# Kernel optimization log

Hardware: AMD Instinct MI355X
Metric: run time of the kernel (lower is better)

Reference implementation:

```python
import jax, jax.numpy as jnp
import numpy as np
from jax import lax

MU = 3.986004418e14   # Earth GM [m^3/s^2]
A_REF = 6378136.3     # reference radius [m]


def _constants(N, dtype):
    """Precompute n1/n2 normalization tables, diagonal aBar values and the
    sub-diagonal coefficient, exactly as in compute_normalization_constants
    and the first loop of compute_aBar (these depend only on N, not on data)."""
    L = N + 2
    l = np.arange(L, dtype=np.float64)[:, None]
    m = np.arange(L, dtype=np.float64)[None, :]
    mask = l >= m + 2
    d1 = np.where(mask, (l - m) * (l + m), 1.0)
    n1 = np.where(mask, np.sqrt((2.0 * l + 1.0) * (2.0 * l - 1.0) / d1), 0.0)
    d2 = np.where(mask, (l + m) * (l - m) * (2.0 * l - 3.0), 1.0)
    num2 = np.where(mask, (l + m - 1.0) * (2.0 * l + 1.0) * (l - m - 1.0), 0.0)
    n2 = np.where(mask, np.sqrt(num2 / d2), 0.0)
    # getK(0)=1, getK(l>0)=2
    k = np.where(np.arange(L) == 0, 1.0, 2.0)
    ls = np.arange(1, L, dtype=np.float64)
    f = np.ones(L)
    f[1:] = np.sqrt((2.0 * ls + 1.0) * k[1:] / (2.0 * ls * k[:-1]))
    diag = np.cumprod(f)                  # aBar[l,l]
    sub = np.zeros(L)
    sub[1:] = np.sqrt(2.0 * ls * k[:-1] / k[1:])  # aBar[l,l-1] = sub[l]*diag[l]*u
    cast = lambda x: jnp.asarray(x, dtype=dtype)
    return cast(n1), cast(n2), cast(diag), cast(sub)


def _forward(inputs, cBar, sBar):
    N = cBar.shape[0] - 3
    L = N + 2
    dt = inputs.dtype
    r, s, t, u = inputs[:, 0], inputs[:, 1], inputs[:, 2], inputs[:, 3]
    B = r.shape[0]
    n1, n2, diag, sub = _constants(N, dt)

    # rhol[b, l] = (mu/r) * (a/r)^l  for l = 0..N  (compute_rhol)
    rho = A_REF / r
    rhol = (MU / r)[:, None] * rho[:, None] ** jnp.arange(N + 1, dtype=dt)  # [B, N+1]

    # rE[m] + i*iM[m] = (s + i t)^m, m = 0..N+1  (compute_rE_iM)
    def trig_step(c, _):
        re, im = c
        nc = (s * re - t * im, s * im + t * re)
        return nc, nc
    init = (jnp.ones_like(s), jnp.zeros_like(s))
    _, (reS, imS) = lax.scan(trig_step, init, None, length=L - 1)
    rE = jnp.concatenate([init[0][None], reS], axis=0).T  # [B, L]
    iM = jnp.concatenate([init[1][None], imS], axis=0).T  # [B, L]

    # rows of aBar for l=0 and l=1
    sqrt3 = jnp.sqrt(jnp.asarray(3.0, dt))
    row0 = jnp.zeros((B, L), dt).at[:, 0].set(1.0)
    row1 = jnp.zeros((B, L), dt).at[:, 1].set(sqrt3)
    row1 = row1.at[:, 0].set(sqrt3 * u)  # aBar[1,0] = sub[1]*diag[1]*u

    cB = cBar[:, :L].astype(dt)
    sB = sBar[:, :L].astype(dt)
    eye = jnp.eye(L, dtype=dt)

    # scan over degree l = 2..N; carry = (aBar row l-1, aBar row l-2)
    xs = (n1[2:N + 1], n2[2:N + 1], cB[2:N + 1], sB[2:N + 1],
          eye[2:N + 1], eye[1:N], diag[2:N + 1], sub[2:N + 1],
          rhol[:, 2:N + 1].T)

    def body(carry, x):
        rl1, rl2 = carry
        n1l, n2l, cl, sl, el, elm1, dl, sbl, rh = x
        # recurrence a[l,m] = u*n1[l,m]*a[l-1,m] - n2[l,m]*a[l-2,m]  (m <= l-2;
        # n1/n2 are zero elsewhere so other entries stay 0 before diag fill)
        row = u[:, None] * (n1l * rl1) - n2l * rl2
        row = row + dl * el + (sbl * dl) * u[:, None] * elm1
        contrib = rh * jnp.sum(row * (cl * rE + sl * iM), axis=1)
        return (row, rl1), contrib

    _, contribs = lax.scan(body, (row1, row0), xs)  # [N-1, B]

    pot1 = rhol[:, 1] * jnp.sum(row1 * (cB[1] * rE + sB[1] * iM), axis=1)
    potential = MU / r + pot1 + contribs.sum(axis=0)
    return (-potential)[:, None]


def setup_inputs() -> dict:
    key = jax.random.key(0)
    B, N = 65536, 64
    k1, k2, k3, k4 = jax.random.split(key, 4)
    d = jax.random.normal(k1, (B, 3), dtype=jnp.float32)
    d = d / jnp.linalg.norm(d, axis=1, keepdims=True)  # (s,t,u) direction cosines
    r = A_REF * (1.0 + jax.random.uniform(k2, (B,), dtype=jnp.float32,
                                          minval=0.05, maxval=1.0))
    inputs = jnp.concatenate([r[:, None], d], axis=1)  # [B,4] = (r,s,t,u)
    cBar = jax.random.normal(k3, (N + 3, N + 3), dtype=jnp.float32) * 1e-3
    sBar = jax.random.normal(k4, (N + 3, N + 3), dtype=jnp.float32) * 1e-3
    return {"inputs": inputs, "cBar": cBar, "sBar": sBar}


def reference(inputs, cBar, sBar):
    return _forward(inputs, cBar, sBar)
```

## Files before the change

### kernel.cpp

```cpp
#include <hip/hip_runtime.h>
#include <math.h>

#define NDEG 64
#define LDCB 67

#define MU_F   398600441800000.0f
#define AREF_F 6378136.3f

#define NSUB 8
#define EPW  64
#define SGRP 72
#define NREC 9

struct Cons4 { float4 v[4]; };

__device__ __forceinline__ double n1d(int l, int m) {
    return sqrt((2.0 * l + 1.0) * (2.0 * l - 1.0) / ((double)(l - m) * (l + m)));
}
__device__ __forceinline__ double n2d(int l, int m) {
    return sqrt(((double)(l + m - 1) * (2 * l + 1) * (l - m - 1)) /
                ((double)(l + m) * (l - m) * (2 * l - 3)));
}

__global__ void pines_setup(const float* __restrict__ cBar,
                            const float* __restrict__ sBar,
                            float4* __restrict__ stream,
                            float4* __restrict__ hrec) {
    int tid = blockIdx.x * blockDim.x + threadIdx.x;
    if (tid < 8 * SGRP * 4) {
        int j = tid / (SGRP * 4);
        int rem = tid % (SGRP * 4);
        int d1 = 15 - 2 * j, d2 = 1 + 2 * j;
        int m = j, base = 0, idx = -1;
        for (int k = 0; k < 8; ++k) {
            int len  = 63 - m;
            int ecap = ((len + 7) >> 3) << 3;
            if (rem < base + ecap) { idx = rem - base; break; }
            base += ecap;
            m += (k & 1) ? d2 : d1;
        }
        float4 v = make_float4(0.0f, 0.0f, 0.0f, 0.0f);
        if (idx >= 0) {
            int l = m + 2 + idx;
            if (l <= NDEG) {
                double g = 1.0;
                for (int t2 = m + 2; t2 <= l; ++t2) g *= n1d(t2, m);
                double nn1   = n1d(l, m);
                double nprev = (l - 1 >= m + 2) ? n1d(l - 1, m) : 1.0;
                double nt2   = n2d(l, m) / (nn1 * nprev);
                v = make_float4((float)nt2,
                                (float)(g * (double)cBar[l * LDCB + m]),
                                (float)(g * (double)sBar[l * LDCB + m]),
                                0.0f);
            }
        }
        stream[tid] = v;
    } else {
        int h = tid - 8 * SGRP * 4;
        if (h < 8 * NREC) {
            int j = h / NREC, k = h % NREC;
            int d1 = 15 - 2 * j, d2 = 1 + 2 * j;
            int m = j;
            for (int kk = 0; kk < k; ++kk) m += (kk & 1) ? d2 : d1;
            float4 a = make_float4(0.0f, 0.0f, 0.0f, 0.0f);
            float4 b = make_float4(0.0f, 0.0f, 0.0f, 0.0f);
            if (m <= NDEG) {
                double diag = 1.0;
                for (int l = 1; l <= m; ++l) {
                    double kp = (l == 1) ? 1.0 : 2.0;
                    diag *= sqrt((2.0 * l + 1.0) * 2.0 / (2.0 * l * kp));
                }
                double sd = 0.0;
                if (m < NDEG) {
                    double kprev = (m == 0) ? 1.0 : 2.0;
                    double f    = sqrt((2.0 * (m + 1) + 1.0) * 2.0 /
                                       (2.0 * (m + 1) * kprev));
                    double sub1 = sqrt((double)(m + 1) * kprev);
                    sd = sub1 * diag * f;
                }
                float cmm = (m >= 1) ? cBar[m * LDCB + m] : 0.0f;
                float smm = (m >= 1) ? sBar[m * LDCB + m] : 0.0f;
                float cb1 = (m < NDEG) ? cBar[(m + 1) * LDCB + m] : 0.0f;
                float sb1 = (m < NDEG) ? sBar[(m + 1) * LDCB + m] : 0.0f;
                a = make_float4((float)diag, (float)sd, cmm, smm);
                b = make_float4(cb1, sb1, 0.0f, 0.0f);
            }
            hrec[h * 2]     = a;
            hrec[h * 2 + 1] = b;
        }
    }
}

__global__ __launch_bounds__(512, 8) void pines_kernel(
        const float4* __restrict__ inputs,
        const float4* __restrict__ stream,
        const float4* __restrict__ hrec,
        float* __restrict__ out, int B) {
    __shared__ float part[NSUB][EPW];

    int t = threadIdx.x;
    int j = __builtin_amdgcn_readfirstlane(t >> 6);
    int e = t & (EPW - 1);
    int elem = blockIdx.x * EPW + e;
    int lelem = elem < B ? elem : (B - 1);

    float4 in = inputs[lelem];
    float r = in.x, ss = in.y, tt = in.z, u = in.w;

    float rho   = AREF_F / r;
    float rho2  = rho * rho;
    float nrho2 = -rho2;
    float ur    = u * rho;

    int d1 = 15 - 2 * j;
    int d2 = 1 + 2 * j;

    auto cpow = [&](int e_, float& re_, float& im_) {
        float br = ss, bi = tt;
        re_ = 1.0f; im_ = 0.0f;
        int ee = e_;
        while (ee) {
            if (ee & 1) {
                float nr = re_ * br - im_ * bi;
                im_ = re_ * bi + im_ * br;
                re_ = nr;
            }
            float sr = br * br - bi * bi;
            bi = 2.0f * br * bi;
            br = sr;
            ee >>= 1;
        }
    };
    auto rpow = [&](int e_) {
        float b = rho, acc = 1.0f;
        int ee = e_;
        while (ee) {
            if (ee & 1) acc *= b;
            b *= b;
            ee >>= 1;
        }
        return acc;
    };

    float re, im;      cpow(j, re, im);
    float s1r, s1i;    cpow(d1, s1r, s1i);
    float s2r, s2i;    cpow(d2, s2r, s2i);
    float rstep1 = rpow(d1);
    float rstep2 = rpow(d2);
    float rho_m  = rpow(j);

    float sum = (j == 0) ? 1.0f : 0.0f;

    const float4* __restrict__ hp = hrec + j * NREC * 2;
    const Cons4*  __restrict__ sp = (const Cons4*)stream + j * SGRP;

    float4 h0 = hp[0];
    float4 h1 = hp[1];

    int m = j, g = 0;
    #pragma unroll 1
    for (int k = 0; k < 8; ++k) {
        int sm = __builtin_amdgcn_readfirstlane(m);
        float4 h0n = hp[2 * k + 2];
        float4 h1n = hp[2 * k + 3];

        float q0 = h0.x * rho_m;
        float sA = q0 * h0.z;
        float sB = q0 * h0.w;
        float q1 = (h0.y * u) * (rho_m * rho);
        sA = fmaf(q1, h1.x, sA);
        sB = fmaf(q1, h1.y, sB);

        int ntr = __builtin_amdgcn_readfirstlane((63 - sm + 7) >> 3);
        #pragma unroll 1
        for (int tr = 0; tr < ntr; ++tr) {
            Cons4 ca = sp[g];
            Cons4 cb = sp[g + 1];
            g += 2;
            #pragma unroll
            for (int q4 = 0; q4 < 4; ++q4) {
                float4 cc = ca.v[q4];
                float t3 = cc.x * q0;
                float t4 = nrho2 * t3;
                float q  = fmaf(ur, q1, t4);
                sA = fmaf(q, cc.y, sA);
                sB = fmaf(q, cc.z, sB);
                q0 = q1; q1 = q;
            }
            #pragma unroll
            for (int q4 = 0; q4 < 4; ++q4) {
                float4 cc = cb.v[q4];
                float t3 = cc.x * q0;
                float t4 = nrho2 * t3;
                float q  = fmaf(ur, q1, t4);
                sA = fmaf(q, cc.y, sA);
                sB = fmaf(q, cc.z, sB);
                q0 = q1; q1 = q;
            }
        }
        sum = fmaf(re, sA, sum);
        sum = fmaf(im, sB, sum);

        if (k & 1) {
            float nr = re * s2r - im * s2i;
            im = re * s2i + im * s2r; re = nr;
            rho_m *= rstep2; m += d2;
        } else {
            float nr = re * s1r - im * s1i;
            im = re * s1i + im * s1r; re = nr;
            rho_m *= rstep1; m += d1;
        }
        h0 = h0n; h1 = h1n;
    }
    {
        float q0 = h0.x * rho_m;
        sum = fmaf(re * q0, h0.z, sum);
        sum = fmaf(im * q0, h0.w, sum);
    }

    part[j][e] = sum;
    __syncthreads();
    if (j == 0) {
        float tot = 0.0f;
        #pragma unroll
        for (int q = 0; q < NSUB; ++q) tot += part[q][e];
        if (elem < B) out[elem] = -(MU_F / r) * tot;
    }
}

extern "C" void kernel_launch(void* const* d_in, const int* in_sizes, int n_in,
                              void* d_out, int out_size, void* d_ws, size_t ws_size,
                              hipStream_t stream_h) {
    const float* inputs = (const float*)d_in[0];
    const float* cBar   = (const float*)d_in[1];
    const float* sBar   = (const float*)d_in[2];
    float* out = (float*)d_out;
    int B = in_sizes[0] / 4;

    float4* strm = (float4*)d_ws;
    float4* hrec = strm + 8 * SGRP * 4;

    hipLaunchKernelGGL(pines_setup, dim3(10), dim3(256), 0, stream_h,
                       cBar, sBar, strm, hrec);

    int blocks = (B + EPW - 1) / EPW;
    hipLaunchKernelGGL(pines_kernel, dim3(blocks), dim3(512), 0, stream_h,
                       (const float4*)inputs, strm, hrec, out, B);
}
```

Baseline: 98.36 us.

## Stage coefficient stream in LDS and compute setup tables with running products

The main kernel now copies each wave's coefficient stream (288 float4 per wave, about 36 KB per block) from global memory into shared memory at block start and reads the inner recurrence constants from LDS instead of scalar/global loads. The setup kernel is restructured so each thread computes a whole segment with a running product of the normalization factors instead of recomputing the product per element, and it launches only two blocks. The large LDS allocation cuts occupancy per CU, and every block pays the copy cost, traded against cheaper per-iteration constant fetches.

```diff
diff --git a/kernel.cpp b/kernel.cpp
--- a/kernel.cpp
+++ b/kernel.cpp
@@ -10,55 +10,17 @@
 #define NSUB 8
 #define EPW  64
 #define SGRP 72
+#define SF4  (SGRP * 4)
 #define NREC 9
-
-struct Cons4 { float4 v[4]; };
-
-__device__ __forceinline__ double n1d(int l, int m) {
-    return sqrt((2.0 * l + 1.0) * (2.0 * l - 1.0) / ((double)(l - m) * (l + m)));
-}
-__device__ __forceinline__ double n2d(int l, int m) {
-    return sqrt(((double)(l + m - 1) * (2 * l + 1) * (l - m - 1)) /
-                ((double)(l + m) * (l - m) * (2 * l - 3)));
-}
 
 __global__ void pines_setup(const float* __restrict__ cBar,
                             const float* __restrict__ sBar,
                             float4* __restrict__ stream,
                             float4* __restrict__ hrec) {
-    int tid = blockIdx.x * blockDim.x + threadIdx.x;
-    if (tid < 8 * SGRP * 4) {
-        int j = tid / (SGRP * 4);
-        int rem = tid % (SGRP * 4);
-        int d1 = 15 - 2 * j, d2 = 1 + 2 * j;
-        int m = j, base = 0, idx = -1;
-        for (int k = 0; k < 8; ++k) {
-            int len  = 63 - m;
-            int ecap = ((len + 7) >> 3) << 3;
-            if (rem < base + ecap) { idx = rem - base; break; }
-            base += ecap;
-            m += (k & 1) ? d2 : d1;
-        }
-        float4 v = make_float4(0.0f, 0.0f, 0.0f, 0.0f);
-        if (idx >= 0) {
-            int l = m + 2 + idx;
-            if (l <= NDEG) {
-                double g = 1.0;
-                for (int t2 = m + 2; t2 <= l; ++t2) g *= n1d(t2, m);
-                double nn1   = n1d(l, m);
-                double nprev = (l - 1 >= m + 2) ? n1d(l - 1, m) : 1.0;
-                double nt2   = n2d(l, m) / (nn1 * nprev);
-                v = make_float4((float)nt2,
-                                (float)(g * (double)cBar[l * LDCB + m]),
-                                (float)(g * (double)sBar[l * LDCB + m]),
-                                0.0f);
-            }
-        }
-        stream[tid] = v;
-    } else {
-        int h = tid - 8 * SGRP * 4;
-        if (h < 8 * NREC) {
-            int j = h / NREC, k = h % NREC;
+    int t = threadIdx.x;
+    if (blockIdx.x == 0) {
+        if (t < 8 * NREC) {
+            int j = t / NREC, k = t % NREC;
             int d1 = 15 - 2 * j, d2 = 1 + 2 * j;
             int m = j;
             for (int kk = 0; kk < k; ++kk) m += (kk & 1) ? d2 : d1;
@@ -85,8 +47,41 @@
                 a = make_float4((float)diag, (float)sd, cmm, smm);
                 b = make_float4(cb1, sb1, 0.0f, 0.0f);
             }
-            hrec[h * 2]     = a;
-            hrec[h * 2 + 1] = b;
+            hrec[t * 2]     = a;
+            hrec[t * 2 + 1] = b;
+        }
+    } else {
+        if (t < 64) {
+            int j = t >> 3, k = t & 7;
+            int d1 = 15 - 2 * j, d2 = 1 + 2 * j;
+            int m = j, base = 0;
+            for (int kk = 0; kk < k; ++kk) {
+                int len = 63 - m;
+                base += ((len + 7) >> 3) << 3;
+                m += (kk & 1) ? d2 : d1;
+            }
+            int len  = 63 - m;
+            int ecap = ((len + 7) >> 3) << 3;
+            float4* __restrict__ dst = stream + j * SF4 + base;
+            double G = 1.0;
+            for (int i = 0; i < ecap; ++i) {
+                float4 v = make_float4(0.0f, 0.0f, 0.0f, 0.0f);
+                if (i < len) {
+                    int l = m + 2 + i;
+                    G *= (2.0 * l + 1.0) * (2.0 * l - 1.0) /
+                         ((double)(l - m) * (l + m));
+                    double g = sqrt(G);
+                    double nt2 = (i == 0)
+                        ? sqrt(1.0 / (2.0 * m + 3.0))
+                        : ((double)(l + m - 1) * (l - m - 1)) /
+                          ((double)(2 * l - 1) * (2 * l - 3));
+                    v = make_float4((float)nt2,
+                                    (float)(g * (double)cBar[l * LDCB + m]),
+                                    (float)(g * (double)sBar[l * LDCB + m]),
+                                    0.0f);
+                }
+                dst[i] = v;
+            }
         }
     }
 }
@@ -96,6 +91,7 @@
         const float4* __restrict__ stream,
         const float4* __restrict__ hrec,
         float* __restrict__ out, int B) {
+    __shared__ float4 sh[8 * SF4];
     __shared__ float part[NSUB][EPW];
 
     int t = threadIdx.x;
@@ -103,6 +99,16 @@
     int e = t & (EPW - 1);
     int elem = blockIdx.x * EPW + e;
     int lelem = elem < B ? elem : (B - 1);
+
+    {
+        const float4* __restrict__ src = stream + j * SF4;
+        float4* __restrict__ dst = sh + j * SF4;
+        #pragma unroll
+        for (int i = 0; i < SF4 / EPW; ++i)
+            dst[e + i * EPW] = src[e + i * EPW];
+        if (e < SF4 - (SF4 / EPW) * EPW + 0) {}
+        if (e < 32) dst[256 + e] = src[256 + e];
+    }
 
     float4 in = inputs[lelem];
     float r = in.x, ss = in.y, tt = in.z, u = in.w;
@@ -152,12 +158,12 @@
     float sum = (j == 0) ? 1.0f : 0.0f;
 
     const float4* __restrict__ hp = hrec + j * NREC * 2;
-    const Cons4*  __restrict__ sp = (const Cons4*)stream + j * SGRP;
+    const float4* __restrict__ wsh = sh + j * SF4;
 
     float4 h0 = hp[0];
     float4 h1 = hp[1];
 
-    int m = j, g = 0;
+    int m = j, gi = 0;
     #pragma unroll 1
     for (int k = 0; k < 8; ++k) {
         int sm = __builtin_amdgcn_readfirstlane(m);
@@ -174,22 +180,24 @@
         int ntr = __builtin_amdgcn_readfirstlane((63 - sm + 7) >> 3);
         #pragma unroll 1
         for (int tr = 0; tr < ntr; ++tr) {
-            Cons4 ca = sp[g];
-            Cons4 cb = sp[g + 1];
-            g += 2;
+            float4 c0 = wsh[gi + 0];
+            float4 c1 = wsh[gi + 1];
+            float4 c2 = wsh[gi + 2];
+            float4 c3 = wsh[gi + 3];
+            float4 c4 = wsh[gi + 4];
+            float4 c5 = wsh[gi + 5];
+            float4 c6 = wsh[gi + 6];
+            float4 c7 = wsh[gi + 7];
+            gi += 8;
             #pragma unroll
-            for (int q4 = 0; q4 < 4; ++q4) {
-                float4 cc = ca.v[q4];
-                float t3 = cc.x * q0;
-                float t4 = nrho2 * t3;
-                float q  = fmaf(ur, q1, t4);
-                sA = fmaf(q, cc.y, sA);
-                sB = fmaf(q, cc.z, sB);
-                q0 = q1; q1 = q;
-            }
-            #pragma unroll
-            for (int q4 = 0; q4 < 4; ++q4) {
-                float4 cc = cb.v[q4];
+            for (int q4 = 0; q4 < 8; ++q4) {
+                float4 cc;
+                switch (q4) {
+                    case 0: cc = c0; break; case 1: cc = c1; break;
+                    case 2: cc = c2; break; case 3: cc = c3; break;
+                    case 4: cc = c4; break; case 5: cc = c5; break;
+                    case 6: cc = c6; break; default: cc = c7; break;
+                }
                 float t3 = cc.x * q0;
                 float t4 = nrho2 * t3;
                 float q  = fmaf(ur, q1, t4);
@@ -238,9 +246,9 @@
     int B = in_sizes[0] / 4;
 
     float4* strm = (float4*)d_ws;
-    float4* hrec = strm + 8 * SGRP * 4;
-
-    hipLaunchKernelGGL(pines_setup, dim3(10), dim3(256), 0, stream_h,
+    float4* hrec = strm + 8 * SF4;
+
+    hipLaunchKernelGGL(pines_setup, dim3(2), dim3(128), 0, stream_h,
                        cBar, sBar, strm, hrec);
 
     int blocks = (B + EPW - 1) / EPW;
```

Result: slower. 109.7 us (+11.6%).

## Pack two elements per lane with float2 math and split orders across 16 waves

Applied to the files above, without the earlier changes.

Each lane now processes two batch elements using 2-wide float vectors, so the compiler can emit packed FP32 instructions. The m-columns are split across 16 waves of 4 columns each (zigzag pairing) instead of 8 waves of 8, in 1024-thread blocks covering 128 elements. The setup kernel now builds the normalization stream with running products in a single block. This raises per-lane register pressure and the block size, which may lower occupancy.

```diff
diff --git a/kernel.cpp b/kernel.cpp
--- a/kernel.cpp
+++ b/kernel.cpp
@@ -7,132 +7,136 @@
 #define MU_F   398600441800000.0f
 #define AREF_F 6378136.3f
 
-#define NSUB 8
+#define NSUB 16
 #define EPW  64
-#define SGRP 72
-#define NREC 9
+#define SMAX 160
+#define NREC 5
+
+typedef float f2 __attribute__((ext_vector_type(2)));
+__device__ __forceinline__ f2 make2(float x) { f2 v; v.x = x; v.y = x; return v; }
 
 struct Cons4 { float4 v[4]; };
 
-__device__ __forceinline__ double n1d(int l, int m) {
-    return sqrt((2.0 * l + 1.0) * (2.0 * l - 1.0) / ((double)(l - m) * (l + m)));
-}
-__device__ __forceinline__ double n2d(int l, int m) {
-    return sqrt(((double)(l + m - 1) * (2 * l + 1) * (l - m - 1)) /
-                ((double)(l + m) * (l - m) * (2 * l - 3)));
+__device__ __forceinline__ int zcol(int j, int k) {
+    switch (k) { case 0: return j; case 1: return 31 - j;
+                 case 2: return 32 + j; default: return 63 - j; }
 }
 
 __global__ void pines_setup(const float* __restrict__ cBar,
                             const float* __restrict__ sBar,
                             float4* __restrict__ stream,
                             float4* __restrict__ hrec) {
-    int tid = blockIdx.x * blockDim.x + threadIdx.x;
-    if (tid < 8 * SGRP * 4) {
-        int j = tid / (SGRP * 4);
-        int rem = tid % (SGRP * 4);
-        int d1 = 15 - 2 * j, d2 = 1 + 2 * j;
-        int m = j, base = 0, idx = -1;
-        for (int k = 0; k < 8; ++k) {
-            int len  = 63 - m;
-            int ecap = ((len + 7) >> 3) << 3;
-            if (rem < base + ecap) { idx = rem - base; break; }
-            base += ecap;
-            m += (k & 1) ? d2 : d1;
-        }
-        float4 v = make_float4(0.0f, 0.0f, 0.0f, 0.0f);
-        if (idx >= 0) {
-            int l = m + 2 + idx;
-            if (l <= NDEG) {
-                double g = 1.0;
-                for (int t2 = m + 2; t2 <= l; ++t2) g *= n1d(t2, m);
-                double nn1   = n1d(l, m);
-                double nprev = (l - 1 >= m + 2) ? n1d(l - 1, m) : 1.0;
-                double nt2   = n2d(l, m) / (nn1 * nprev);
+    int t = threadIdx.x;
+    if (t < 64) {
+        int j = t >> 2, c = t & 3;
+        int base = 0;
+        for (int cc = 0; cc < c; ++cc) {
+            int len = 63 - zcol(j, cc);
+            base += ((len + 7) >> 3) << 3;
+        }
+        int m    = zcol(j, c);
+        int len  = 63 - m;
+        int ecap = ((len + 7) >> 3) << 3;
+        float4* __restrict__ dst = stream + j * SMAX + base;
+        double G = 1.0;
+        for (int i = 0; i < ecap; ++i) {
+            float4 v = make_float4(0.0f, 0.0f, 0.0f, 0.0f);
+            if (i < len) {
+                int l = m + 2 + i;
+                G *= (2.0 * l + 1.0) * (2.0 * l - 1.0) /
+                     ((double)(l - m) * (l + m));
+                double g = sqrt(G);
+                double nt2 = (i == 0)
+                    ? sqrt(1.0 / (2.0 * m + 3.0))
+                    : ((double)(l + m - 1) * (l - m - 1)) /
+                      ((double)(2 * l - 1) * (2 * l - 3));
                 v = make_float4((float)nt2,
                                 (float)(g * (double)cBar[l * LDCB + m]),
                                 (float)(g * (double)sBar[l * LDCB + m]),
                                 0.0f);
             }
-        }
-        stream[tid] = v;
-    } else {
-        int h = tid - 8 * SGRP * 4;
-        if (h < 8 * NREC) {
-            int j = h / NREC, k = h % NREC;
-            int d1 = 15 - 2 * j, d2 = 1 + 2 * j;
-            int m = j;
-            for (int kk = 0; kk < k; ++kk) m += (kk & 1) ? d2 : d1;
-            float4 a = make_float4(0.0f, 0.0f, 0.0f, 0.0f);
-            float4 b = make_float4(0.0f, 0.0f, 0.0f, 0.0f);
-            if (m <= NDEG) {
-                double diag = 1.0;
-                for (int l = 1; l <= m; ++l) {
-                    double kp = (l == 1) ? 1.0 : 2.0;
-                    diag *= sqrt((2.0 * l + 1.0) * 2.0 / (2.0 * l * kp));
-                }
-                double sd = 0.0;
-                if (m < NDEG) {
-                    double kprev = (m == 0) ? 1.0 : 2.0;
-                    double f    = sqrt((2.0 * (m + 1) + 1.0) * 2.0 /
-                                       (2.0 * (m + 1) * kprev));
-                    double sub1 = sqrt((double)(m + 1) * kprev);
-                    sd = sub1 * diag * f;
-                }
-                float cmm = (m >= 1) ? cBar[m * LDCB + m] : 0.0f;
-                float smm = (m >= 1) ? sBar[m * LDCB + m] : 0.0f;
-                float cb1 = (m < NDEG) ? cBar[(m + 1) * LDCB + m] : 0.0f;
-                float sb1 = (m < NDEG) ? sBar[(m + 1) * LDCB + m] : 0.0f;
-                a = make_float4((float)diag, (float)sd, cmm, smm);
-                b = make_float4(cb1, sb1, 0.0f, 0.0f);
-            }
-            hrec[h * 2]     = a;
-            hrec[h * 2 + 1] = b;
-        }
-    }
-}
-
-__global__ __launch_bounds__(512, 8) void pines_kernel(
+            dst[i] = v;
+        }
+    } else if (t < 64 + NSUB * NREC) {
+        int h = t - 64;
+        int j = h / NREC, k = h % NREC;
+        int m = (k < 4) ? zcol(j, k) : ((j == 0) ? 64 : 99);
+        float4 a = make_float4(0.0f, 0.0f, 0.0f, 0.0f);
+        float4 b = make_float4(0.0f, 0.0f, 0.0f, 0.0f);
+        if (m <= NDEG) {
+            double diag = 1.0;
+            for (int l = 1; l <= m; ++l) {
+                double kp = (l == 1) ? 1.0 : 2.0;
+                diag *= sqrt((2.0 * l + 1.0) * 2.0 / (2.0 * l * kp));
+            }
+            double sd = 0.0;
+            if (m < NDEG) {
+                double kprev = (m == 0) ? 1.0 : 2.0;
+                double f    = sqrt((2.0 * (m + 1) + 1.0) * 2.0 /
+                                   (2.0 * (m + 1) * kprev));
+                double sub1 = sqrt((double)(m + 1) * kprev);
+                sd = sub1 * diag * f;
+            }
+            float cmm = (m >= 1) ? cBar[m * LDCB + m] : 0.0f;
+            float smm = (m >= 1) ? sBar[m * LDCB + m] : 0.0f;
+            float cb1 = (m < NDEG) ? cBar[(m + 1) * LDCB + m] : 0.0f;
+            float sb1 = (m < NDEG) ? sBar[(m + 1) * LDCB + m] : 0.0f;
+            a = make_float4((float)diag, (float)sd, cmm, smm);
+            b = make_float4(cb1, sb1, 0.0f, 0.0f);
+        }
+        hrec[h * 2]     = a;
+        hrec[h * 2 + 1] = b;
+    }
+}
+
+__global__ __launch_bounds__(1024, 8) void pines_kernel(
         const float4* __restrict__ inputs,
         const float4* __restrict__ stream,
         const float4* __restrict__ hrec,
         float* __restrict__ out, int B) {
-    __shared__ float part[NSUB][EPW];
+    __shared__ f2 part[NSUB][EPW];
 
     int t = threadIdx.x;
     int j = __builtin_amdgcn_readfirstlane(t >> 6);
     int e = t & (EPW - 1);
-    int elem = blockIdx.x * EPW + e;
-    int lelem = elem < B ? elem : (B - 1);
-
-    float4 in = inputs[lelem];
-    float r = in.x, ss = in.y, tt = in.z, u = in.w;
-
-    float rho   = AREF_F / r;
-    float rho2  = rho * rho;
-    float nrho2 = -rho2;
-    float ur    = u * rho;
-
-    int d1 = 15 - 2 * j;
+    int base = blockIdx.x * 128;
+    int e0 = base + e;       if (e0 >= B) e0 = B - 1;
+    int e1 = base + 64 + e;  if (e1 >= B) e1 = B - 1;
+
+    float4 inA = inputs[e0];
+    float4 inB = inputs[e1];
+    f2 r, sv, tv, u;
+    r.x = inA.x; r.y = inB.x;
+    sv.x = inA.y; sv.y = inB.y;
+    tv.x = inA.z; tv.y = inB.z;
+    u.x = inA.w; u.y = inB.w;
+
+    f2 rho   = AREF_F / r;
+    f2 rho2  = rho * rho;
+    f2 nrho2 = -rho2;
+    f2 ur    = u * rho;
+
+    int d1 = 31 - 2 * j;
     int d2 = 1 + 2 * j;
 
-    auto cpow = [&](int e_, float& re_, float& im_) {
-        float br = ss, bi = tt;
-        re_ = 1.0f; im_ = 0.0f;
+    auto cpow = [&](int e_, f2& re_, f2& im_) {
+        f2 br = sv, bi = tv;
+        re_ = make2(1.0f); im_ = make2(0.0f);
         int ee = e_;
         while (ee) {
             if (ee & 1) {
-                float nr = re_ * br - im_ * bi;
+                f2 nr = re_ * br - im_ * bi;
                 im_ = re_ * bi + im_ * br;
                 re_ = nr;
             }
-            float sr = br * br - bi * bi;
+            f2 sr = br * br - bi * bi;
             bi = 2.0f * br * bi;
             br = sr;
             ee >>= 1;
         }
     };
     auto rpow = [&](int e_) {
-        float b = rho, acc = 1.0f;
+        f2 b = rho, acc = make2(1.0f);
         int ee = e_;
         while (ee) {
             if (ee & 1) acc *= b;
@@ -142,34 +146,34 @@
         return acc;
     };
 
-    float re, im;      cpow(j, re, im);
-    float s1r, s1i;    cpow(d1, s1r, s1i);
-    float s2r, s2i;    cpow(d2, s2r, s2i);
-    float rstep1 = rpow(d1);
-    float rstep2 = rpow(d2);
-    float rho_m  = rpow(j);
-
-    float sum = (j == 0) ? 1.0f : 0.0f;
+    f2 re, im;      cpow(j, re, im);
+    f2 s1r, s1i;    cpow(d1, s1r, s1i);
+    f2 s2r, s2i;    cpow(d2, s2r, s2i);
+    f2 rstep1 = rpow(d1);
+    f2 rstep2 = rpow(d2);
+    f2 rho_m  = rpow(j);
+
+    f2 sum = (j == 0) ? make2(1.0f) : make2(0.0f);
 
     const float4* __restrict__ hp = hrec + j * NREC * 2;
-    const Cons4*  __restrict__ sp = (const Cons4*)stream + j * SGRP;
+    const Cons4*  __restrict__ sp = (const Cons4*)(stream + j * SMAX);
 
     float4 h0 = hp[0];
     float4 h1 = hp[1];
 
-    int m = j, g = 0;
+    int g = 0;
     #pragma unroll 1
-    for (int k = 0; k < 8; ++k) {
-        int sm = __builtin_amdgcn_readfirstlane(m);
+    for (int k = 0; k < 4; ++k) {
+        int sm = __builtin_amdgcn_readfirstlane(zcol(j, k));
         float4 h0n = hp[2 * k + 2];
         float4 h1n = hp[2 * k + 3];
 
-        float q0 = h0.x * rho_m;
-        float sA = q0 * h0.z;
-        float sB = q0 * h0.w;
-        float q1 = (h0.y * u) * (rho_m * rho);
-        sA = fmaf(q1, h1.x, sA);
-        sB = fmaf(q1, h1.y, sB);
+        f2 q0 = h0.x * rho_m;
+        f2 sA = q0 * h0.z;
+        f2 sB = q0 * h0.w;
+        f2 q1 = (h0.y * u) * (rho_m * rho);
+        sA += q1 * h1.x;
+        sB += q1 * h1.y;
 
         int ntr = __builtin_amdgcn_readfirstlane((63 - sm + 7) >> 3);
         #pragma unroll 1
@@ -180,51 +184,55 @@
             #pragma unroll
             for (int q4 = 0; q4 < 4; ++q4) {
                 float4 cc = ca.v[q4];
-                float t3 = cc.x * q0;
-                float t4 = nrho2 * t3;
-                float q  = fmaf(ur, q1, t4);
-                sA = fmaf(q, cc.y, sA);
-                sB = fmaf(q, cc.z, sB);
+                f2 t4 = nrho2 * (cc.x * q0);
+                f2 q  = ur * q1 + t4;
+                sA += q * cc.y;
+                sB += q * cc.z;
                 q0 = q1; q1 = q;
             }
             #pragma unroll
             for (int q4 = 0; q4 < 4; ++q4) {
                 float4 cc = cb.v[q4];
-                float t3 = cc.x * q0;
-                float t4 = nrho2 * t3;
-                float q  = fmaf(ur, q1, t4);
-                sA = fmaf(q, cc.y, sA);
-                sB = fmaf(q, cc.z, sB);
+                f2 t4 = nrho2 * (cc.x * q0);
+                f2 q  = ur * q1 + t4;
+                sA += q * cc.y;
+                sB += q * cc.z;
                 q0 = q1; q1 = q;
             }
         }
-        sum = fmaf(re, sA, sum);
-        sum = fmaf(im, sB, sum);
-
-        if (k & 1) {
-            float nr = re * s2r - im * s2i;
-            im = re * s2i + im * s2r; re = nr;
-            rho_m *= rstep2; m += d2;
-        } else {
-            float nr = re * s1r - im * s1i;
-            im = re * s1i + im * s1r; re = nr;
-            rho_m *= rstep1; m += d1;
+        sum += re * sA + im * sB;
+
+        if (k < 3) {
+            if (k & 1) {
+                f2 nr = re * s2r - im * s2i;
+                im = re * s2i + im * s2r; re = nr;
+                rho_m *= rstep2;
+            } else {
+                f2 nr = re * s1r - im * s1i;
+                im = re * s1i + im * s1r; re = nr;
+                rho_m *= rstep1;
+            }
         }
         h0 = h0n; h1 = h1n;
     }
     {
-        float q0 = h0.x * rho_m;
-        sum = fmaf(re * q0, h0.z, sum);
-        sum = fmaf(im * q0, h0.w, sum);
+        f2 nr = sv * re - tv * im;
+        f2 ni = sv * im + tv * re;
+        re = nr; im = ni;
+        rho_m *= rho;
+        f2 q0 = h0.x * rho_m;
+        sum += (re * q0) * h0.z + (im * q0) * h0.w;
     }
 
     part[j][e] = sum;
     __syncthreads();
     if (j == 0) {
-        float tot = 0.0f;
+        f2 tot = make2(0.0f);
         #pragma unroll
         for (int q = 0; q < NSUB; ++q) tot += part[q][e];
-        if (elem < B) out[elem] = -(MU_F / r) * tot;
+        f2 res = -(MU_F / r) * tot;
+        if (base + e < B)      out[base + e]      = res.x;
+        if (base + 64 + e < B) out[base + 64 + e] = res.y;
     }
 }
 
@@ -238,12 +246,12 @@
     int B = in_sizes[0] / 4;
 
     float4* strm = (float4*)d_ws;
-    float4* hrec = strm + 8 * SGRP * 4;
-
-    hipLaunchKernelGGL(pines_setup, dim3(10), dim3(256), 0, stream_h,
+    float4* hrec = strm + NSUB * SMAX;
+
+    hipLaunchKernelGGL(pines_setup, dim3(1), dim3(256), 0, stream_h,
                        cBar, sBar, strm, hrec);
 
-    int blocks = (B + EPW - 1) / EPW;
-    hipLaunchKernelGGL(pines_kernel, dim3(blocks), dim3(512), 0, stream_h,
+    int blocks = (B + 127) / 128;
+    hipLaunchKernelGGL(pines_kernel, dim3(blocks), dim3(1024), 0, stream_h,
                        (const float4*)inputs, strm, hrec, out, B);
 }
```

New measurement: 93.18 us. 1.06x faster.

## Pad coefficient stream to fixed per-segment lengths and fully unroll recurrence loops

Applied to the files above, without the earlier changes.

The coefficient stream is re-laid out so each of the 8 per-wave segments has a fixed compile-time padded length (64, 56, …, 8) at fixed offsets. This lets the main kernel fully unroll the order loop and the inner recurrence with constant load offsets, removing runtime trip counts, readfirstlane calls and pointer bookkeeping. The setup kernel is also simplified to one block, with a running-product normalization computed serially per chain. The cost is extra zero-padded recurrence steps for some waves (every wave now does 288 steps), much larger unrolled code, and possibly more register pressure.

```diff
diff --git a/kernel.cpp b/kernel.cpp
--- a/kernel.cpp
+++ b/kernel.cpp
@@ -9,85 +9,96 @@
 
 #define NSUB 8
 #define EPW  64
-#define SGRP 72
 #define NREC 9
-
-struct Cons4 { float4 v[4]; };
-
-__device__ __forceinline__ double n1d(int l, int m) {
-    return sqrt((2.0 * l + 1.0) * (2.0 * l - 1.0) / ((double)(l - m) * (l + m)));
-}
-__device__ __forceinline__ double n2d(int l, int m) {
-    return sqrt(((double)(l + m - 1) * (2 * l + 1) * (l - m - 1)) /
-                ((double)(l + m) * (l - m) * (2 * l - 3)));
+#define SF4  288
+
+#define PAD0 64
+#define PAD1 56
+#define PAD2 48
+#define PAD3 40
+#define PAD4 32
+#define PAD5 24
+#define PAD6 16
+#define PAD7 8
+#define OFF0 0
+#define OFF1 64
+#define OFF2 120
+#define OFF3 168
+#define OFF4 208
+#define OFF5 240
+#define OFF6 264
+#define OFF7 280
+
+struct alignas(64) Cons4 { float4 v[4]; };
+
+__device__ __forceinline__ int zig8(int j, int k) {
+    switch (k) { case 0: return j;      case 1: return 15 - j;
+                 case 2: return 16 + j; case 3: return 31 - j;
+                 case 4: return 32 + j; case 5: return 47 - j;
+                 case 6: return 48 + j; default: return 63 - j; }
 }
 
 __global__ void pines_setup(const float* __restrict__ cBar,
                             const float* __restrict__ sBar,
                             float4* __restrict__ stream,
                             float4* __restrict__ hrec) {
-    int tid = blockIdx.x * blockDim.x + threadIdx.x;
-    if (tid < 8 * SGRP * 4) {
-        int j = tid / (SGRP * 4);
-        int rem = tid % (SGRP * 4);
-        int d1 = 15 - 2 * j, d2 = 1 + 2 * j;
-        int m = j, base = 0, idx = -1;
-        for (int k = 0; k < 8; ++k) {
-            int len  = 63 - m;
-            int ecap = ((len + 7) >> 3) << 3;
-            if (rem < base + ecap) { idx = rem - base; break; }
-            base += ecap;
-            m += (k & 1) ? d2 : d1;
-        }
-        float4 v = make_float4(0.0f, 0.0f, 0.0f, 0.0f);
-        if (idx >= 0) {
-            int l = m + 2 + idx;
-            if (l <= NDEG) {
-                double g = 1.0;
-                for (int t2 = m + 2; t2 <= l; ++t2) g *= n1d(t2, m);
-                double nn1   = n1d(l, m);
-                double nprev = (l - 1 >= m + 2) ? n1d(l - 1, m) : 1.0;
-                double nt2   = n2d(l, m) / (nn1 * nprev);
+    const int PADK[8] = {PAD0,PAD1,PAD2,PAD3,PAD4,PAD5,PAD6,PAD7};
+    const int OFFK[8] = {OFF0,OFF1,OFF2,OFF3,OFF4,OFF5,OFF6,OFF7};
+    int t = threadIdx.x;
+    if (t < 64) {
+        int j = t >> 3, k = t & 7;
+        int m    = zig8(j, k);
+        int len  = 63 - m;
+        int ecap = PADK[k];
+        float4* __restrict__ dst = stream + j * SF4 + OFFK[k];
+        double G = 1.0;
+        for (int i = 0; i < ecap; ++i) {
+            float4 v = make_float4(0.0f, 0.0f, 0.0f, 0.0f);
+            if (i < len) {
+                int l = m + 2 + i;
+                G *= (2.0 * l + 1.0) * (2.0 * l - 1.0) /
+                     ((double)(l - m) * (l + m));
+                double g = sqrt(G);
+                double nt2 = (i == 0)
+                    ? sqrt(1.0 / (2.0 * m + 3.0))
+                    : ((double)(l + m - 1) * (l - m - 1)) /
+                      ((double)(2 * l - 1) * (2 * l - 3));
                 v = make_float4((float)nt2,
                                 (float)(g * (double)cBar[l * LDCB + m]),
                                 (float)(g * (double)sBar[l * LDCB + m]),
                                 0.0f);
             }
-        }
-        stream[tid] = v;
-    } else {
-        int h = tid - 8 * SGRP * 4;
-        if (h < 8 * NREC) {
-            int j = h / NREC, k = h % NREC;
-            int d1 = 15 - 2 * j, d2 = 1 + 2 * j;
-            int m = j;
-            for (int kk = 0; kk < k; ++kk) m += (kk & 1) ? d2 : d1;
-            float4 a = make_float4(0.0f, 0.0f, 0.0f, 0.0f);
-            float4 b = make_float4(0.0f, 0.0f, 0.0f, 0.0f);
-            if (m <= NDEG) {
-                double diag = 1.0;
-                for (int l = 1; l <= m; ++l) {
-                    double kp = (l == 1) ? 1.0 : 2.0;
-                    diag *= sqrt((2.0 * l + 1.0) * 2.0 / (2.0 * l * kp));
-                }
-                double sd = 0.0;
-                if (m < NDEG) {
-                    double kprev = (m == 0) ? 1.0 : 2.0;
-                    double f    = sqrt((2.0 * (m + 1) + 1.0) * 2.0 /
-                                       (2.0 * (m + 1) * kprev));
-                    double sub1 = sqrt((double)(m + 1) * kprev);
-                    sd = sub1 * diag * f;
-                }
-                float cmm = (m >= 1) ? cBar[m * LDCB + m] : 0.0f;
-                float smm = (m >= 1) ? sBar[m * LDCB + m] : 0.0f;
-                float cb1 = (m < NDEG) ? cBar[(m + 1) * LDCB + m] : 0.0f;
-                float sb1 = (m < NDEG) ? sBar[(m + 1) * LDCB + m] : 0.0f;
-                a = make_float4((float)diag, (float)sd, cmm, smm);
-                b = make_float4(cb1, sb1, 0.0f, 0.0f);
-            }
-            hrec[h * 2]     = a;
-            hrec[h * 2 + 1] = b;
-        }
+            dst[i] = v;
+        }
+    } else if (t < 64 + NSUB * NREC) {
+        int h = t - 64;
+        int j = h / NREC, k = h % NREC;
+        int m = (k < 8) ? zig8(j, k) : ((j == 0) ? 64 : 99);
+        float4 a = make_float4(0.0f, 0.0f, 0.0f, 0.0f);
+        float4 b = make_float4(0.0f, 0.0f, 0.0f, 0.0f);
+        if (m <= NDEG) {
+            double diag = 1.0;
+            for (int l = 1; l <= m; ++l) {
+                double kp = (l == 1) ? 1.0 : 2.0;
+                diag *= sqrt((2.0 * l + 1.0) * 2.0 / (2.0 * l * kp));
+            }
+            double sd = 0.0;
+            if (m < NDEG) {
+                double kprev = (m == 0) ? 1.0 : 2.0;
+                double f    = sqrt((2.0 * (m + 1) + 1.0) * 2.0 /
+                                   (2.0 * (m + 1) * kprev));
+                double sub1 = sqrt((double)(m + 1) * kprev);
+                sd = sub1 * diag * f;
+            }
+            float cmm = (m >= 1) ? cBar[m * LDCB + m] : 0.0f;
+            float smm = (m >= 1) ? sBar[m * LDCB + m] : 0.0f;
+            float cb1 = (m < NDEG) ? cBar[(m + 1) * LDCB + m] : 0.0f;
+            float sb1 = (m < NDEG) ? sBar[(m + 1) * LDCB + m] : 0.0f;
+            a = make_float4((float)diag, (float)sd, cmm, smm);
+            b = make_float4(cb1, sb1, 0.0f, 0.0f);
+        }
+        hrec[h * 2]     = a;
+        hrec[h * 2 + 1] = b;
     }
 }
 
@@ -96,6 +107,8 @@
         const float4* __restrict__ stream,
         const float4* __restrict__ hrec,
         float* __restrict__ out, int B) {
+    const int PADK[8] = {PAD0,PAD1,PAD2,PAD3,PAD4,PAD5,PAD6,PAD7};
+    const int OFFK[8] = {OFF0,OFF1,OFF2,OFF3,OFF4,OFF5,OFF6,OFF7};
     __shared__ float part[NSUB][EPW];
 
     int t = threadIdx.x;
@@ -152,17 +165,12 @@
     float sum = (j == 0) ? 1.0f : 0.0f;
 
     const float4* __restrict__ hp = hrec + j * NREC * 2;
-    const Cons4*  __restrict__ sp = (const Cons4*)stream + j * SGRP;
-
-    float4 h0 = hp[0];
-    float4 h1 = hp[1];
-
-    int m = j, g = 0;
-    #pragma unroll 1
+    const Cons4*  __restrict__ sp = (const Cons4*)(stream + j * SF4);
+
+    #pragma unroll
     for (int k = 0; k < 8; ++k) {
-        int sm = __builtin_amdgcn_readfirstlane(m);
-        float4 h0n = hp[2 * k + 2];
-        float4 h1n = hp[2 * k + 3];
+        float4 h0 = hp[2 * k];
+        float4 h1 = hp[2 * k + 1];
 
         float q0 = h0.x * rho_m;
         float sA = q0 * h0.z;
@@ -171,12 +179,11 @@
         sA = fmaf(q1, h1.x, sA);
         sB = fmaf(q1, h1.y, sB);
 
-        int ntr = __builtin_amdgcn_readfirstlane((63 - sm + 7) >> 3);
-        #pragma unroll 1
+        const int ntr = PADK[k] >> 3;
+        #pragma unroll
         for (int tr = 0; tr < ntr; ++tr) {
-            Cons4 ca = sp[g];
-            Cons4 cb = sp[g + 1];
-            g += 2;
+            Cons4 ca = sp[(OFFK[k] >> 2) + 2 * tr];
+            Cons4 cb = sp[(OFFK[k] >> 2) + 2 * tr + 1];
             #pragma unroll
             for (int q4 = 0; q4 < 4; ++q4) {
                 float4 cc = ca.v[q4];
@@ -204,15 +211,15 @@
         if (k & 1) {
             float nr = re * s2r - im * s2i;
             im = re * s2i + im * s2r; re = nr;
-            rho_m *= rstep2; m += d2;
+            rho_m *= rstep2;
         } else {
             float nr = re * s1r - im * s1i;
             im = re * s1i + im * s1r; re = nr;
-            rho_m *= rstep1; m += d1;
-        }
-        h0 = h0n; h1 = h1n;
+            rho_m *= rstep1;
+        }
     }
     {
+        float4 h0 = hp[16];
         float q0 = h0.x * rho_m;
         sum = fmaf(re * q0, h0.z, sum);
         sum = fmaf(im * q0, h0.w, sum);
@@ -238,9 +245,9 @@
     int B = in_sizes[0] / 4;
 
     float4* strm = (float4*)d_ws;
-    float4* hrec = strm + 8 * SGRP * 4;
-
-    hipLaunchKernelGGL(pines_setup, dim3(10), dim3(256), 0, stream_h,
+    float4* hrec = strm + NSUB * SF4;
+
+    hipLaunchKernelGGL(pines_setup, dim3(1), dim3(256), 0, stream_h,
                        cBar, sBar, strm, hrec);
 
     int blocks = (B + EPW - 1) / EPW;
```

Measured after the change: 96.71 us. Within noise of the previous version (-1.7%).
